# Performance work log

Measured on AMD Instinct MI355X. Metric: run time of the kernel, lower is better.

Reference implementation:

```python
import jax, jax.numpy as jnp
import numpy as np
import math

L, B, T, E, HQ, HKV, V = 6, 4, 1024, 1024, 16, 4, 32000
D = E // HQ          # head dim = 64
G = HQ // HKV        # group size = 4
EKV = E // G         # kv proj dim = 256


def setup_inputs() -> dict:
    key = jax.random.key(0)
    ks = jax.random.split(key, 16)
    def n(k, shape):
        return jax.random.normal(k, shape, jnp.float32) * 0.02
    return dict(
        idx=jax.random.randint(ks[0], (B, T), 0, V),
        wte=n(ks[1], (V, E)),
        Wq=n(ks[2], (L, E, E)), bq=jnp.zeros((L, E), jnp.float32),
        Wk=n(ks[3], (L, EKV, E)), bk=jnp.zeros((L, EKV), jnp.float32),
        Wv=n(ks[4], (L, EKV, E)), bv=jnp.zeros((L, EKV), jnp.float32),
        Wo=n(ks[5], (L, E, E)), bo=jnp.zeros((L, E), jnp.float32),
        ln1_w=jnp.ones((L, E), jnp.float32), ln1_b=jnp.zeros((L, E), jnp.float32),
        ln2_w=jnp.ones((L, E), jnp.float32), ln2_b=jnp.zeros((L, E), jnp.float32),
        Wfc=n(ks[6], (L, 4 * E, E)), bfc=jnp.zeros((L, 4 * E), jnp.float32),
        Wproj=n(ks[7], (L, E, 4 * E)), bproj=jnp.zeros((L, E), jnp.float32),
        lnf_w=jnp.ones((E,), jnp.float32), lnf_b=jnp.zeros((E,), jnp.float32),
        lm_head=n(ks[8], (V, E)),
    )


def _ln(x, w, b):
    m = x.mean(-1, keepdims=True)
    v = ((x - m) ** 2).mean(-1, keepdims=True)
    return (x - m) * jax.lax.rsqrt(v + 1e-5) * w + b


def _gelu_new(x):
    c = math.sqrt(2.0 / math.pi)
    return 0.5 * x * (1.0 + jnp.tanh(c * (x + 0.044715 * x ** 3)))


def _rope_tables(t, d):
    # positions start at 1; thetas = base^(-2*(i-1)/d), i = 1..d/2
    pos = jnp.arange(1, t + 1, dtype=jnp.float32)
    thetas = 10000.0 ** (-2.0 * jnp.arange(d // 2, dtype=jnp.float32) / d)
    ang = pos[:, None] * thetas                      # [t, d/2]
    cos = jnp.concatenate([jnp.cos(ang)] * 2, -1)    # [t, d]
    sin = jnp.concatenate([jnp.sin(ang)] * 2, -1)
    return cos, sin


def _apply_rope(x, cos, sin):
    # x: [b, h, t, d]; x_cos = x; x_sin = concat(-right, left)
    x1, x2 = x[..., : D // 2], x[..., D // 2:]
    return x * cos + jnp.concatenate([-x2, x1], -1) * sin


def _gpt_forward(idx, wte, Wq, bq, Wk, bk, Wv, bv, Wo, bo,
                 ln1_w, ln1_b, ln2_w, ln2_b, Wfc, bfc, Wproj, bproj,
                 lnf_w, lnf_b, lm_head):
    cos, sin = _rope_tables(T, D)
    mask = jnp.tril(jnp.ones((T, T), bool))          # causal
    scale = 1.0 / math.sqrt(D)
    x = wte[idx]                                     # [B, T, E]
    for l in range(L):
        h = _ln(x, ln1_w[l], ln1_b[l])
        q = (h @ Wq[l].T + bq[l]).reshape(B, T, HQ, D).transpose(0, 2, 1, 3)
        k = (h @ Wk[l].T + bk[l]).reshape(B, T, HKV, D).transpose(0, 2, 1, 3)
        v = (h @ Wv[l].T + bv[l]).reshape(B, T, HKV, D).transpose(0, 2, 1, 3)
        q = _apply_rope(q, cos, sin)
        k = _apply_rope(k, cos, sin)
        q = q.reshape(B, HKV, G, T, D)               # kv-major head grouping
        att = jnp.einsum('bhgqd,bhkd->bhgqk', q, k) * scale
        att = jnp.where(mask, att, -jnp.inf)
        att = jax.nn.softmax(att, axis=-1)
        y = jnp.einsum('bhgqk,bhkd->bhgqd', att, v)
        y = y.transpose(0, 3, 1, 2, 4).reshape(B, T, E)   # b q (h g d)
        x = x + (y @ Wo[l].T + bo[l])
        h2 = _ln(x, ln2_w[l], ln2_b[l])
        ff = _gelu_new(h2 @ Wfc[l].T + bfc[l]) @ Wproj[l].T + bproj[l]
        x = x + ff
    x = _ln(x, lnf_w, lnf_b)
    return x @ lm_head.T                             # [B, T, V] logits


def reference(idx, wte, Wq, bq, Wk, bk, Wv, bv, Wo, bo,
              ln1_w, ln1_b, ln2_w, ln2_b, Wfc, bfc, Wproj, bproj,
              lnf_w, lnf_b, lm_head):
    return _gpt_forward(idx, wte, Wq, bq, Wk, bk, Wv, bv, Wo, bo,
                        ln1_w, ln1_b, ln2_w, ln2_b, Wfc, bfc, Wproj, bproj,
                        lnf_w, lnf_b, lm_head)
```

## Files before the change

kernel.cpp:

```cpp
#include <hip/hip_runtime.h>

#define Lz 6
#define Bz 4
#define Tz 1024
#define Ez 1024
#define HQz 16
#define HKVz 4
#define Dz 64
#define EKVz 256
#define Vz 32000
#define FFz 4096
#define QKVz 1536

typedef __attribute__((ext_vector_type(4))) float f32x4;
typedef __attribute__((ext_vector_type(8))) short short8;
typedef unsigned short ushort_t;

__device__ inline ushort_t f2b(float f) {
  union { float f; unsigned u; } x; x.f = f;
  unsigned r = x.u + 0x7fffu + ((x.u >> 16) & 1u);
  return (ushort_t)(r >> 16);
}
__device__ inline float b2f(ushort_t u) {
  union { unsigned u; float f; } x; x.u = ((unsigned)u) << 16;
  return x.f;
}
__device__ inline unsigned packbf(float lo, float hi) {
  return (unsigned)f2b(lo) | ((unsigned)f2b(hi) << 16);
}

__device__ inline void gload16(const void* g, void* l) {
  __builtin_amdgcn_global_load_lds(
      (const __attribute__((address_space(1))) void*)g,
      (__attribute__((address_space(3))) void*)l, 16, 0, 0);
}

template<int BIAS, int GELU, int WF32>
__global__ __launch_bounds__(512, 2) void gemm_bt256(
    const ushort_t* __restrict__ A, const ushort_t* __restrict__ Bw,
    const float* __restrict__ bias,
    float* __restrict__ Cf, ushort_t* __restrict__ Cb,
    int M, int N, int K)
{
  __shared__ ushort_t sA[2][2][128 * 64];
  __shared__ ushort_t sB[2][2][128 * 64];
  const int tid = threadIdx.x;
  const int lane = tid & 63, wid = tid >> 6;
  const int wr = wid >> 2, wc = wid & 3;
  const int l15 = lane & 15, l4 = lane >> 4;

  const int gx = gridDim.x;
  const int nwg = gx * gridDim.y;
  const int orig = blockIdx.y * gx + blockIdx.x;
  const int qq = nwg >> 3, rr = nwg & 7;
  const int xcd = orig & 7, loc = orig >> 3;
  const int swz = (xcd < rr) ? (xcd * (qq + 1) + loc)
                             : (rr * (qq + 1) + (xcd - rr) * qq + loc);
  const int bm = swz % gx, bn = swz / gx;

  const int NT = K >> 6;

  auto stage = [&](const ushort_t* src, int row_base, int k0, ushort_t* dst) {
#pragma unroll
    for (int i = 0; i < 2; ++i) {
      int s = i * 512 + tid;
      int row = s >> 3, jp = s & 7;
      int jlog = jp ^ (row & 7);
      gload16(src + (size_t)(row_base + row) * K + k0 + jlog * 8, (char*)dst + s * 16);
    }
  };

  stage(A,  bm * 256,       0, &sA[0][0][0]);
  stage(A,  bm * 256 + 128, 0, &sA[0][1][0]);
  stage(Bw, bn * 256,       0, &sB[0][0][0]);
  stage(Bw, bn * 256 + 128, 0, &sB[0][1][0]);
  stage(A,  bm * 256,       64, &sA[1][0][0]);
  stage(A,  bm * 256 + 128, 64, &sA[1][1][0]);
  stage(Bw, bn * 256,       64, &sB[1][0][0]);
  stage(Bw, bn * 256 + 128, 64, &sB[1][1][0]);
  asm volatile("s_waitcnt vmcnt(8)" ::: "memory");
  __builtin_amdgcn_sched_barrier(0);
  __builtin_amdgcn_s_barrier();
  __builtin_amdgcn_sched_barrier(0);

  f32x4 acc[8][4] = {};
  const int axc = l15 & 7;

  for (int t = 0; t < NT; ++t) {
    const int b = t & 1;
    const ushort_t* pA = &sA[b][wr][0];
    const ushort_t* pB = &sB[b][wc >> 1][(wc & 1) * 64 * 64];
    short8 aF[8][2], bF[4][2];

#pragma unroll
    for (int mt = 0; mt < 4; ++mt)
#pragma unroll
      for (int ks = 0; ks < 2; ++ks)
        aF[mt][ks] = *(const short8*)&pA[(mt * 16 + l15) * 64 + (((ks << 2) + l4) ^ axc) * 8];
#pragma unroll
    for (int nt = 0; nt < 4; ++nt)
      bF[nt][0] = *(const short8*)&pB[(nt * 16 + l15) * 64 + (l4 ^ axc) * 8];
    __builtin_amdgcn_s_setprio(1);
#pragma unroll
    for (int mt = 0; mt < 4; ++mt)
#pragma unroll
      for (int nt = 0; nt < 4; ++nt)
        acc[mt][nt] = __builtin_amdgcn_mfma_f32_16x16x32_bf16(aF[mt][0], bF[nt][0], acc[mt][nt], 0, 0, 0);
    __builtin_amdgcn_s_setprio(0);

#pragma unroll
    for (int mt = 4; mt < 8; ++mt)
#pragma unroll
      for (int ks = 0; ks < 2; ++ks)
        aF[mt][ks] = *(const short8*)&pA[(mt * 16 + l15) * 64 + (((ks << 2) + l4) ^ axc) * 8];
#pragma unroll
    for (int nt = 0; nt < 4; ++nt)
      bF[nt][1] = *(const short8*)&pB[(nt * 16 + l15) * 64 + ((4 + l4) ^ axc) * 8];
    __builtin_amdgcn_s_setprio(1);
#pragma unroll
    for (int mt = 0; mt < 4; ++mt)
#pragma unroll
      for (int nt = 0; nt < 4; ++nt)
        acc[mt][nt] = __builtin_amdgcn_mfma_f32_16x16x32_bf16(aF[mt][1], bF[nt][1], acc[mt][nt], 0, 0, 0);
    __builtin_amdgcn_s_setprio(0);

    asm volatile("s_waitcnt lgkmcnt(0)" ::: "memory");
    __builtin_amdgcn_sched_barrier(0);
    __builtin_amdgcn_s_barrier();
    __builtin_amdgcn_sched_barrier(0);

    const bool pf = (t + 2 < NT);
    if (pf) {
      const int k2 = (t + 2) << 6;
      stage(Bw, bn * 256,       k2, &sB[b][0][0]);
      stage(Bw, bn * 256 + 128, k2, &sB[b][1][0]);
    }
    __builtin_amdgcn_s_setprio(1);
#pragma unroll
    for (int mt = 4; mt < 8; ++mt)
#pragma unroll
      for (int nt = 0; nt < 4; ++nt)
        acc[mt][nt] = __builtin_amdgcn_mfma_f32_16x16x32_bf16(aF[mt][0], bF[nt][0], acc[mt][nt], 0, 0, 0);
    __builtin_amdgcn_s_setprio(0);

    if (pf) {
      const int k2 = (t + 2) << 6;
      stage(A, bm * 256,       k2, &sA[b][0][0]);
      stage(A, bm * 256 + 128, k2, &sA[b][1][0]);
    }
    __builtin_amdgcn_s_setprio(1);
#pragma unroll
    for (int mt = 4; mt < 8; ++mt)
#pragma unroll
      for (int nt = 0; nt < 4; ++nt)
        acc[mt][nt] = __builtin_amdgcn_mfma_f32_16x16x32_bf16(aF[mt][1], bF[nt][1], acc[mt][nt], 0, 0, 0);
    __builtin_amdgcn_s_setprio(0);

    if (t + 1 < NT) {
      if (pf) { asm volatile("s_waitcnt vmcnt(8)" ::: "memory"); }
      else    { asm volatile("s_waitcnt vmcnt(0)" ::: "memory"); }
      __builtin_amdgcn_sched_barrier(0);
      __builtin_amdgcn_s_barrier();
      __builtin_amdgcn_sched_barrier(0);
    }
  }

#pragma unroll
  for (int mt = 0; mt < 8; ++mt) {
#pragma unroll
    for (int nt = 0; nt < 4; ++nt) {
      const int col = bn * 256 + wc * 64 + nt * 16 + l15;
#pragma unroll
      for (int i = 0; i < 4; ++i) {
        const int row = bm * 256 + wr * 128 + mt * 16 + l4 * 4 + i;
        float v = acc[mt][nt][i];
        if (BIAS) v += bias[col];
        if (GELU) {
          float x = v;
          v = 0.5f * x * (1.f + tanhf(0.7978845608028654f * (x + 0.044715f * x * x * x)));
        }
        const size_t o = (size_t)row * N + col;
        if (WF32) Cf[o] = v; else Cb[o] = f2b(v);
      }
    }
  }
}

template<int BIAS, int RES, int GELU, int WF32, int WBF16, int ROPE>
__global__ __launch_bounds__(256) void gemm_bt(
    const ushort_t* __restrict__ A, const ushort_t* __restrict__ Bw,
    const float* __restrict__ bias, const float* __restrict__ res,
    float* __restrict__ Cf, ushort_t* __restrict__ Cb,
    const float2* __restrict__ tab,
    int M, int N, int K)
{
  __shared__ ushort_t sA[2][128 * 32];
  __shared__ ushort_t sB[2][128 * 32];
  const int tid = threadIdx.x;
  const int lane = tid & 63, wid = tid >> 6;
  const int wm = wid >> 1, wn = wid & 1;
  const int l15 = lane & 15, l4 = lane >> 4;

  const int gx = gridDim.x;
  const int nwg = gx * gridDim.y;
  const int orig = blockIdx.y * gx + blockIdx.x;
  const int qq = nwg >> 3, rr = nwg & 7;
  const int xcd = orig & 7, loc = orig >> 3;
  const int swz = (xcd < rr) ? (xcd * (qq + 1) + loc)
                             : (rr * (qq + 1) + (xcd - rr) * qq + loc);
  const int bm = swz % gx, bn = swz / gx;

  f32x4 acc[4][4] = {};
  const int nK = K >> 5;

#pragma unroll
  for (int j = 0; j < 2; ++j) {
    int s = wid * 128 + j * 64 + lane;
    int row = s >> 2, c8 = (s & 3) << 3;
    gload16(A + (size_t)(bm * 128 + row) * K + c8, (char*)&sA[0][0] + s * 16);
    gload16(Bw + (size_t)(bn * 128 + row) * K + c8, (char*)&sB[0][0] + s * 16);
  }
  __syncthreads();

  int cur = 0;
  for (int kt = 0; kt < nK; ++kt) {
    if (kt + 1 < nK) {
      const int k0 = (kt + 1) << 5;
      const int nb = cur ^ 1;
#pragma unroll
      for (int j = 0; j < 2; ++j) {
        int s = wid * 128 + j * 64 + lane;
        int row = s >> 2, c8 = (s & 3) << 3;
        gload16(A + (size_t)(bm * 128 + row) * K + k0 + c8, (char*)&sA[nb][0] + s * 16);
        gload16(Bw + (size_t)(bn * 128 + row) * K + k0 + c8, (char*)&sB[nb][0] + s * 16);
      }
    }
    short8 aF[4], bF[4];
#pragma unroll
    for (int mt = 0; mt < 4; ++mt)
      aF[mt] = *(const short8*)&sA[cur][(wm * 64 + mt * 16 + l15) * 32 + l4 * 8];
#pragma unroll
    for (int nt = 0; nt < 4; ++nt)
      bF[nt] = *(const short8*)&sB[cur][(wn * 64 + nt * 16 + l15) * 32 + l4 * 8];
#pragma unroll
    for (int mt = 0; mt < 4; ++mt)
#pragma unroll
      for (int nt = 0; nt < 4; ++nt)
        acc[mt][nt] = __builtin_amdgcn_mfma_f32_16x16x32_bf16(aF[mt], bF[nt], acc[mt][nt], 0, 0, 0);
    __syncthreads();
    cur ^= 1;
  }

  if (ROPE) {
    const int col0 = bn * 128 + wn * 64;
    const bool isv = (col0 >= 1280);
#pragma unroll
    for (int mt = 0; mt < 4; ++mt) {
#pragma unroll
      for (int i = 0; i < 4; ++i) {
        const int row = bm * 128 + wm * 64 + mt * 16 + l4 * 4 + i;
        const int t = row & (Tz - 1);
        if (isv) {
#pragma unroll
          for (int nt = 0; nt < 4; ++nt) {
            const int col = col0 + nt * 16 + l15;
            Cb[(size_t)row * N + col] = f2b(acc[mt][nt][i] + bias[col]);
          }
        } else {
#pragma unroll
          for (int nt = 0; nt < 2; ++nt) {
            const int col = col0 + nt * 16 + l15;
            const int jj = nt * 16 + l15;
            const float2 cs = tab[t * 32 + jj];
            const float x1 = acc[mt][nt][i] + bias[col];
            const float x2 = acc[mt][nt + 2][i] + bias[col + 32];
            Cb[(size_t)row * N + col]      = f2b(x1 * cs.x - x2 * cs.y);
            Cb[(size_t)row * N + col + 32] = f2b(x2 * cs.x + x1 * cs.y);
          }
        }
      }
    }
    return;
  }

#pragma unroll
  for (int mt = 0; mt < 4; ++mt) {
#pragma unroll
    for (int nt = 0; nt < 4; ++nt) {
      const int col = bn * 128 + wn * 64 + nt * 16 + l15;
#pragma unroll
      for (int i = 0; i < 4; ++i) {
        const int row = bm * 128 + wm * 64 + mt * 16 + l4 * 4 + i;
        float v = acc[mt][nt][i];
        if (BIAS) v += bias[col];
        if (GELU) {
          float t = v;
          v = 0.5f * t * (1.f + tanhf(0.7978845608028654f * (t + 0.044715f * t * t * t)));
        }
        const size_t o = (size_t)row * N + col;
        if (RES) v += res[o];
        if (WF32) Cf[o] = v;
        if (WBF16) Cb[o] = f2b(v);
      }
    }
  }
}

__global__ __launch_bounds__(256, 4) void attn_k(
    const ushort_t* __restrict__ qkv, const ushort_t* __restrict__ vt,
    ushort_t* __restrict__ y)
{
  __shared__ ushort_t sK[2][64 * 64];
  __shared__ ushort_t sV[2][64 * 64];
  __shared__ unsigned sPu[4][512];
  const int qt = blockIdx.x;
  const int bh = blockIdx.y;
  const int b = bh >> 4, h = bh & 15, hk = h >> 2;
  const int tid = threadIdx.x, lane = tid & 63, wid = tid >> 6;
  const int l15 = lane & 15, l4 = lane >> 4;
  const int qrow0 = qt * 64 + wid * 16;
  const int qg = qrow0 + l15;
  const int xr = l15 & 7;

  short8 aQ[2];
#pragma unroll
  for (int ks = 0; ks < 2; ++ks)
    aQ[ks] = *(const short8*)&qkv[(size_t)(b * Tz + qrow0 + l15) * QKVz + h * 64 + ks * 32 + l4 * 8];

  float m = -1e30f, lsum = 0.f;
  f32x4 o[4] = {};

  const int ntile = qt + 1;

#pragma unroll
  for (int j = 0; j < 2; ++j) {
    int s = wid * 128 + j * 64 + lane;
    int row = s >> 3, jp = s & 7, jlog = jp ^ (row & 7);
    gload16(qkv + (size_t)(b * Tz + row) * QKVz + Ez + hk * 64 + jlog * 8, (char*)&sK[0][0] + s * 16);
    gload16(vt + (size_t)((b * HKVz + hk) * 64 + row) * Tz + jlog * 8, (char*)&sV[0][0] + s * 16);
  }

  for (int t = 0; t < ntile; ++t) {
    asm volatile("s_waitcnt vmcnt(0)" ::: "memory");
    __syncthreads();
    if (t + 1 < ntile) {
      const int nb = (t + 1) & 1;
#pragma unroll
      for (int j = 0; j < 2; ++j) {
        int s = wid * 128 + j * 64 + lane;
        int row = s >> 3, jp = s & 7, jlog = jp ^ (row & 7);
        gload16(qkv + (size_t)(b * Tz + (t + 1) * 64 + row) * QKVz + Ez + hk * 64 + jlog * 8,
                (char*)&sK[nb][0] + s * 16);
        gload16(vt + (size_t)((b * HKVz + hk) * 64 + row) * Tz + (t + 1) * 64 + jlog * 8,
                (char*)&sV[nb][0] + s * 16);
      }
    }
    const ushort_t* K = &sK[t & 1][0];
    const ushort_t* V = &sV[t & 1][0];

    f32x4 sacc[4] = {};
#pragma unroll
    for (int nt = 0; nt < 4; ++nt) {
#pragma unroll
      for (int ks = 0; ks < 2; ++ks) {
        short8 aK = *(const short8*)&K[(nt * 16 + l15) * 64 + (((ks << 2) + l4) ^ xr) * 8];
        sacc[nt] = __builtin_amdgcn_mfma_f32_16x16x32_bf16(aK, aQ[ks], sacc[nt], 0, 0, 0);
      }
    }

    float sv[4][4];
    float pmax = -1e30f;
#pragma unroll
    for (int nt = 0; nt < 4; ++nt)
#pragma unroll
      for (int i = 0; i < 4; ++i) {
        int key = t * 64 + nt * 16 + l4 * 4 + i;
        float s = sacc[nt][i] * 0.125f;
        if (key > qg) s = -1e30f;
        sv[nt][i] = s;
        pmax = fmaxf(pmax, s);
      }
    pmax = fmaxf(pmax, __shfl_xor(pmax, 16));
    pmax = fmaxf(pmax, __shfl_xor(pmax, 32));
    const float mnew = fmaxf(m, pmax);
    const float corr = __expf(m - mnew);
    float psum = 0.f;
#pragma unroll
    for (int nt = 0; nt < 4; ++nt)
#pragma unroll
      for (int i = 0; i < 4; ++i) {
        float p = __expf(sv[nt][i] - mnew);
        sv[nt][i] = p;
        psum += p;
      }
    psum += __shfl_xor(psum, 16);
    psum += __shfl_xor(psum, 32);
    lsum = lsum * corr + psum;
    m = mnew;
#pragma unroll
    for (int dt = 0; dt < 4; ++dt) o[dt] *= corr;

#pragma unroll
    for (int nt = 0; nt < 4; ++nt) {
      uint2 u;
      u.x = packbf(sv[nt][0], sv[nt][1]);
      u.y = packbf(sv[nt][2], sv[nt][3]);
      *(uint2*)&sPu[wid][l15 * 32 + (((nt * 2 + (l4 >> 1)) ^ xr) << 2) + ((l4 & 1) << 1)] = u;
    }
    short8 aP[2];
#pragma unroll
    for (int ks = 0; ks < 2; ++ks)
      aP[ks] = *(const short8*)&sPu[wid][l15 * 32 + ((((ks << 2) + l4) ^ xr) << 2)];

#pragma unroll
    for (int dt = 0; dt < 4; ++dt) {
#pragma unroll
      for (int ks = 0; ks < 2; ++ks) {
        short8 aV = *(const short8*)&V[(dt * 16 + l15) * 64 + (((ks << 2) + l4) ^ xr) * 8];
        o[dt] = __builtin_amdgcn_mfma_f32_16x16x32_bf16(aV, aP[ks], o[dt], 0, 0, 0);
      }
    }
  }

  const float inv = 1.f / lsum;
  const size_t yrow = (size_t)(b * Tz + qrow0 + l15) * Ez + h * 64;
#pragma unroll
  for (int dt = 0; dt < 4; ++dt) {
    ushort4 w;
    w.x = f2b(o[dt][0] * inv);
    w.y = f2b(o[dt][1] * inv);
    w.z = f2b(o[dt][2] * inv);
    w.w = f2b(o[dt][3] * inv);
    *(ushort4*)&y[yrow + dt * 16 + l4 * 4] = w;
  }
}

__global__ __launch_bounds__(256) void vtrans_k(
    const ushort_t* __restrict__ qkv, ushort_t* __restrict__ vt)
{
  __shared__ ushort_t tile[64][72];
  const int tt = blockIdx.x, bh = blockIdx.y;
  const int b = bh >> 2, hk = bh & 3;
  const int tid = threadIdx.x;
  {
    const int r = tid >> 2, c0 = (tid & 3) * 16;
    const ushort_t* src = qkv + (size_t)(b * Tz + tt * 64 + r) * QKVz + 1280 + hk * 64 + c0;
    *(short8*)&tile[r][c0] = *(const short8*)src;
    *(short8*)&tile[r][c0 + 8] = *(const short8*)(src + 8);
  }
  __syncthreads();
  {
    const int d = tid >> 2, t0 = (tid & 3) * 16;
    ushort_t* dst = vt + (size_t)((b * HKVz + hk) * 64 + d) * Tz + tt * 64 + t0;
    short8 o0, o1;
#pragma unroll
    for (int ii = 0; ii < 8; ++ii) { o0[ii] = (short)tile[t0 + ii][d]; o1[ii] = (short)tile[t0 + 8 + ii][d]; }
    *(short8*)dst = o0;
    *(short8*)(dst + 8) = o1;
  }
}

__global__ __launch_bounds__(256) void ln_bf16(
    const float* __restrict__ x, const float* __restrict__ w,
    const float* __restrict__ b, ushort_t* __restrict__ out)
{
  __shared__ float red[8];
  const int row = blockIdx.x, tid = threadIdx.x;
  float4 vv = *(const float4*)&x[(size_t)row * Ez + tid * 4];
  float s = vv.x + vv.y + vv.z + vv.w;
  float sq = vv.x * vv.x + vv.y * vv.y + vv.z * vv.z + vv.w * vv.w;
#pragma unroll
  for (int off = 1; off < 64; off <<= 1) { s += __shfl_xor(s, off); sq += __shfl_xor(sq, off); }
  if ((tid & 63) == 0) { red[(tid >> 6) * 2] = s; red[(tid >> 6) * 2 + 1] = sq; }
  __syncthreads();
  const float ts = red[0] + red[2] + red[4] + red[6];
  const float tq = red[1] + red[3] + red[5] + red[7];
  const float mean = ts * (1.f / Ez);
  const float var = tq * (1.f / Ez) - mean * mean;
  const float rstd = rsqrtf(var + 1e-5f);
  float4 wv = *(const float4*)&w[tid * 4];
  float4 bv = *(const float4*)&b[tid * 4];
  ushort4 ov;
  ov.x = f2b((vv.x - mean) * rstd * wv.x + bv.x);
  ov.y = f2b((vv.y - mean) * rstd * wv.y + bv.y);
  ov.z = f2b((vv.z - mean) * rstd * wv.z + bv.z);
  ov.w = f2b((vv.w - mean) * rstd * wv.w + bv.w);
  *(ushort4*)&out[(size_t)row * Ez + tid * 4] = ov;
}

__global__ __launch_bounds__(256) void embed_k(
    const int* __restrict__ idx, const float* __restrict__ wte, float* __restrict__ x)
{
  int i = blockIdx.x * 256 + threadIdx.x;
  int row = i >> 8, c = (i & 255) << 2;
  *(float4*)&x[(size_t)row * Ez + c] = *(const float4*)&wte[(size_t)idx[row] * Ez + c];
}

__global__ __launch_bounds__(256) void cvt_bf16(
    const float* __restrict__ in, ushort_t* __restrict__ out, int n)
{
  int i = (blockIdx.x * 256 + threadIdx.x) * 4;
  if (i >= n) return;
  float4 v = *(const float4*)&in[i];
  ushort4 o;
  o.x = f2b(v.x); o.y = f2b(v.y); o.z = f2b(v.z); o.w = f2b(v.w);
  *(ushort4*)&out[i] = o;
}

__global__ __launch_bounds__(256) void cvt_layer(
    const float* __restrict__ Wq, const float* __restrict__ Wk,
    const float* __restrict__ Wv, const float* __restrict__ Wo_,
    const float* __restrict__ Wfc_, const float* __restrict__ Wpj_,
    ushort_t* __restrict__ wqkv, ushort_t* __restrict__ wo,
    ushort_t* __restrict__ wfc, ushort_t* __restrict__ wpj)
{
  int i = (blockIdx.x * 256 + threadIdx.x) * 4;
  const float* src; ushort_t* dst; int off;
  if (i < 1048576)       { src = Wq;   dst = wqkv;           off = i; }
  else if (i < 1310720)  { src = Wk;   dst = wqkv + 1048576; off = i - 1048576; }
  else if (i < 1572864)  { src = Wv;   dst = wqkv + 1310720; off = i - 1310720; }
  else if (i < 2621440)  { src = Wo_;  dst = wo;             off = i - 1572864; }
  else if (i < 6815744)  { src = Wfc_; dst = wfc;            off = i - 2621440; }
  else                   { src = Wpj_; dst = wpj;            off = i - 6815744; }
  float4 v = *(const float4*)&src[off];
  ushort4 o;
  o.x = f2b(v.x); o.y = f2b(v.y); o.z = f2b(v.z); o.w = f2b(v.w);
  *(ushort4*)&dst[off] = o;
}

__global__ __launch_bounds__(256) void rope_tab_k(float2* __restrict__ tab)
{
  int i = blockIdx.x * 256 + threadIdx.x;
  int t = i >> 5, j = i & 31;
  float theta = powf(10000.0f, -(float)j / 32.0f);
  float ang = (float)(t + 1) * theta;
  tab[i] = make_float2(cosf(ang), sinf(ang));
}

__global__ __launch_bounds__(256) void biascat_all(
    const float* __restrict__ bq, const float* __restrict__ bk,
    const float* __restrict__ bv, float* __restrict__ out)
{
  int i = blockIdx.x * 256 + threadIdx.x;
  int l = i / QKVz, j = i - l * QKVz;
  float v = (j < Ez) ? bq[l * Ez + j]
          : ((j < Ez + EKVz) ? bk[l * EKVz + j - Ez] : bv[l * EKVz + j - Ez - EKVz]);
  out[i] = v;
}

template<int BIAS, int RES, int GELU, int WF32, int WBF16, int ROPE = 0>
static void launch_gemm(const ushort_t* A, const ushort_t* Bw, const float* bias,
                        const float* res, float* Cf, ushort_t* Cb, const float* tab,
                        int M, int N, int K, hipStream_t s)
{
  dim3 g(M / 128, N / 128);
  gemm_bt<BIAS, RES, GELU, WF32, WBF16, ROPE><<<g, 256, 0, s>>>(
      A, Bw, bias, res, Cf, Cb, (const float2*)tab, M, N, K);
}

extern "C" void kernel_launch(void* const* d_in, const int* in_sizes, int n_in,
                              void* d_out, int out_size, void* d_ws, size_t ws_size,
                              hipStream_t stream)
{
  (void)in_sizes; (void)n_in; (void)out_size; (void)ws_size;
  const int*   idx   = (const int*)d_in[0];
  const float* wte   = (const float*)d_in[1];
  const float* Wq    = (const float*)d_in[2];
  const float* bq    = (const float*)d_in[3];
  const float* Wk    = (const float*)d_in[4];
  const float* bk    = (const float*)d_in[5];
  const float* Wv    = (const float*)d_in[6];
  const float* bv    = (const float*)d_in[7];
  const float* Wo    = (const float*)d_in[8];
  const float* bo    = (const float*)d_in[9];
  const float* ln1w  = (const float*)d_in[10];
  const float* ln1b  = (const float*)d_in[11];
  const float* ln2w  = (const float*)d_in[12];
  const float* ln2b  = (const float*)d_in[13];
  const float* Wfc   = (const float*)d_in[14];
  const float* bfc   = (const float*)d_in[15];
  const float* Wproj = (const float*)d_in[16];
  const float* bproj = (const float*)d_in[17];
  const float* lnfw  = (const float*)d_in[18];
  const float* lnfb  = (const float*)d_in[19];
  const float* lmh   = (const float*)d_in[20];
  float* out = (float*)d_out;

  char* ws = (char*)d_ws;
  size_t off = 0;
  auto alloc = [&](size_t bytes) -> void* {
    void* p = ws + off;
    off += (bytes + 255) & ~(size_t)255;
    return p;
  };
  ushort_t* wbuf  = (ushort_t*)alloc((size_t)Vz * Ez * 2);
  float*    x     = (float*)alloc((size_t)Bz * Tz * Ez * 4);
  ushort_t* hb    = (ushort_t*)alloc((size_t)Bz * Tz * Ez * 2);
  ushort_t* qkvb  = (ushort_t*)alloc((size_t)Bz * Tz * QKVz * 2);
  ushort_t* vtb   = (ushort_t*)alloc((size_t)Bz * HKVz * 64 * Tz * 2);
  ushort_t* yb    = (ushort_t*)alloc((size_t)Bz * Tz * Ez * 2);
  ushort_t* ffb   = (ushort_t*)alloc((size_t)Bz * Tz * FFz * 2);
  float*    tab   = (float*)alloc((size_t)Tz * 32 * 2 * 4);
  float*    qbia  = (float*)alloc((size_t)Lz * QKVz * 4);

  ushort_t* wqkv = wbuf;
  ushort_t* wo   = wqkv + (size_t)QKVz * Ez;
  ushort_t* wfc  = wo + (size_t)Ez * Ez;
  ushort_t* wpj  = wfc + (size_t)FFz * Ez;

  const int M = Bz * Tz;

  rope_tab_k<<<Tz * 32 / 256, 256, 0, stream>>>((float2*)tab);
  biascat_all<<<Lz * QKVz / 256, 256, 0, stream>>>(bq, bk, bv, qbia);
  embed_k<<<Bz * Tz, 256, 0, stream>>>(idx, wte, x);

  for (int l = 0; l < Lz; ++l) {
    ln_bf16<<<M, 256, 0, stream>>>(x, ln1w + l * Ez, ln1b + l * Ez, hb);
    cvt_layer<<<10752, 256, 0, stream>>>(
        Wq + (size_t)l * Ez * Ez, Wk + (size_t)l * EKVz * Ez, Wv + (size_t)l * EKVz * Ez,
        Wo + (size_t)l * Ez * Ez, Wfc + (size_t)l * FFz * Ez, Wproj + (size_t)l * Ez * FFz,
        wqkv, wo, wfc, wpj);
    launch_gemm<1, 0, 0, 0, 1, 1>(hb, wqkv, qbia + l * QKVz, nullptr, nullptr, qkvb, tab,
                                  M, QKVz, Ez, stream);
    vtrans_k<<<dim3(Tz / 64, Bz * HKVz), 256, 0, stream>>>(qkvb, vtb);
    attn_k<<<dim3(Tz / 64, Bz * HQz), 256, 0, stream>>>(qkvb, vtb, yb);
    launch_gemm<1, 1, 0, 1, 0>(yb, wo, bo + l * Ez, x, x, nullptr, nullptr, M, Ez, Ez, stream);
    ln_bf16<<<M, 256, 0, stream>>>(x, ln2w + l * Ez, ln2b + l * Ez, hb);
    {
      dim3 g(M / 256, FFz / 256);
      gemm_bt256<1, 1, 0><<<g, 512, 0, stream>>>(hb, wfc, bfc + l * FFz, nullptr, ffb, M, FFz, Ez);
    }
    launch_gemm<1, 1, 0, 1, 0>(ffb, wpj, bproj + l * Ez, x, x, nullptr, nullptr, M, Ez, FFz, stream);
  }
  ln_bf16<<<M, 256, 0, stream>>>(x, lnfw, lnfb, hb);
  cvt_bf16<<<(Vz * Ez / 4 + 255) / 256, 256, 0, stream>>>(lmh, wbuf, Vz * Ez);
  {
    dim3 g(M / 256, Vz / 256);
    gemm_bt256<0, 0, 1><<<g, 512, 0, stream>>>(hb, wbuf, nullptr, out, nullptr, M, Vz, Ez);
  }
}
```

Baseline: 1.945 ms.

## Add 8-wave pipelined LM-head GEMM and reverse attention tile order

```diff
diff --git a/kernel.cpp b/kernel.cpp
--- a/kernel.cpp
+++ b/kernel.cpp
@@ -186,6 +186,156 @@
   }
 }
 
+__global__ __launch_bounds__(512, 2) void gemm_lmh8(
+    const ushort_t* __restrict__ A, const ushort_t* __restrict__ Bw,
+    float* __restrict__ Cf, int M, int N, int K)
+{
+  __shared__ ushort_t sA[2][2][128 * 64];
+  __shared__ ushort_t sB[2][2][128 * 64];
+  const int tid = threadIdx.x;
+  const int lane = tid & 63, wid = tid >> 6;
+  const int wr = wid >> 2, wc = wid & 3;
+  const int l15 = lane & 15, l4 = lane >> 4;
+  const int axc = l15 & 7;
+
+  const int gx = gridDim.x;
+  const int nwg = gx * gridDim.y;
+  const int orig = blockIdx.y * gx + blockIdx.x;
+  const int qq = nwg >> 3, rr = nwg & 7;
+  const int xcd = orig & 7, loc = orig >> 3;
+  const int swz = (xcd < rr) ? (xcd * (qq + 1) + loc)
+                             : (rr * (qq + 1) + (xcd - rr) * qq + loc);
+  const int bm = swz % gx, bn = swz / gx;
+
+  const int NT = K >> 6, NI = NT >> 1;
+
+  auto stage = [&](const ushort_t* src, int row_base, int k0, ushort_t* dst) {
+#pragma unroll
+    for (int i = 0; i < 2; ++i) {
+      int s = i * 512 + tid;
+      int row = s >> 3, jp = s & 7;
+      int jlog = jp ^ (row & 7);
+      gload16(src + (size_t)(row_base + row) * K + k0 + jlog * 8, (char*)dst + s * 16);
+    }
+  };
+
+  f32x4 acc[8][4] = {};
+  short8 aF[4][2], bF[4][2];
+
+#define FEN asm volatile("" ::: "memory")
+#define BARR do { FEN; __builtin_amdgcn_s_barrier(); FEN; } while (0)
+#define LGKM0 do { asm volatile("s_waitcnt lgkmcnt(0)" ::: "memory"); \
+                   __builtin_amdgcn_sched_barrier(0); } while (0)
+#define LGKM8 asm volatile("s_waitcnt lgkmcnt(8)" ::: "memory")
+#define VMW(nimm) asm volatile("s_waitcnt vmcnt(" #nimm ")" ::: "memory")
+#define LDA4(base, mt0) do { \
+  const ushort_t* _p = (base); \
+  _Pragma("unroll") for (int _j = 0; _j < 4; ++_j) \
+  _Pragma("unroll") for (int _k = 0; _k < 2; ++_k) \
+    aF[_j][_k] = *(const short8*)&_p[(((mt0) + _j) * 16 + l15) * 64 + ((((_k << 2) + l4)) ^ axc) * 8]; \
+} while (0)
+#define LDB2(base, nt0) do { \
+  const ushort_t* _p = (base); \
+  _Pragma("unroll") for (int _j = 0; _j < 2; ++_j) \
+  _Pragma("unroll") for (int _k = 0; _k < 2; ++_k) \
+    bF[(nt0) + _j][_k] = *(const short8*)&_p[(((nt0) + _j) * 16 + l15) * 64 + ((((_k << 2) + l4)) ^ axc) * 8]; \
+} while (0)
+#define MM16(mt0, nt0) do { \
+  __builtin_amdgcn_s_setprio(1); \
+  _Pragma("unroll") for (int _j = 0; _j < 4; ++_j) \
+  _Pragma("unroll") for (int _n = 0; _n < 2; ++_n) \
+  _Pragma("unroll") for (int _k = 0; _k < 2; ++_k) \
+    acc[(mt0) + _j][(nt0) + _n] = __builtin_amdgcn_mfma_f32_16x16x32_bf16( \
+        aF[_j][_k], bF[(nt0) + _n][_k], acc[(mt0) + _j][(nt0) + _n], 0, 0, 0); \
+  __builtin_amdgcn_s_setprio(0); \
+} while (0)
+
+  stage(A,  bm * 256,       0,  &sA[0][0][0]);
+  stage(A,  bm * 256 + 128, 0,  &sA[0][1][0]);
+  stage(Bw, bn * 256,       0,  &sB[0][0][0]);
+  stage(Bw, bn * 256 + 128, 0,  &sB[0][1][0]);
+  stage(Bw, bn * 256,       64, &sB[1][0][0]);
+  stage(Bw, bn * 256 + 128, 64, &sB[1][1][0]);
+  VMW(4);
+  BARR;
+
+  for (int i = 0; i < NI; ++i) {
+    const bool pf = (2 * i + 2 < NT);
+    const int kA  = (2 * i + 1) << 6;
+    const int kB0 = (2 * i + 2) << 6;
+    const int kB1 = (2 * i + 3) << 6;
+    const ushort_t* pA0 = &sA[0][wr][0];
+    const ushort_t* pA1 = &sA[1][wr][0];
+    const ushort_t* pB0 = &sB[0][wc >> 1][(wc & 1) * 64 * 64];
+    const ushort_t* pB1 = &sB[1][wc >> 1][(wc & 1) * 64 * 64];
+
+    stage(A, bm * 256, kA, &sA[1][0][0]);
+    LDA4(pA0, 0); LDB2(pB0, 0);
+    LGKM8;
+    BARR; LGKM0;
+    MM16(0, 0);
+    BARR;
+    stage(A, bm * 256 + 128, kA, &sA[1][1][0]);
+    LDB2(pB0, 2);
+    BARR; LGKM0;
+    MM16(0, 2);
+    BARR;
+    if (pf) stage(Bw, bn * 256, kB0, &sB[0][0][0]);
+    LDA4(pA0, 4);
+    BARR; LGKM0;
+    MM16(4, 0);
+    BARR;
+    if (pf) { stage(Bw, bn * 256 + 128, kB0, &sB[0][1][0]); VMW(4); }
+    else    { VMW(0); }
+    BARR;
+    MM16(4, 2);
+    BARR;
+    if (pf) stage(A, bm * 256, kB0, &sA[0][0][0]);
+    LDA4(pA1, 0); LDB2(pB1, 0);
+    LGKM8;
+    BARR; LGKM0;
+    MM16(0, 0);
+    BARR;
+    if (pf) stage(A, bm * 256 + 128, kB0, &sA[0][1][0]);
+    LDB2(pB1, 2);
+    BARR; LGKM0;
+    MM16(0, 2);
+    BARR;
+    if (pf) stage(Bw, bn * 256, kB1, &sB[1][0][0]);
+    LDA4(pA1, 4);
+    BARR; LGKM0;
+    MM16(4, 0);
+    BARR;
+    if (pf) { stage(Bw, bn * 256 + 128, kB1, &sB[1][1][0]); VMW(4); }
+    else    { VMW(0); }
+    BARR;
+    MM16(4, 2);
+    BARR;
+  }
+
+#undef FEN
+#undef BARR
+#undef LGKM0
+#undef LGKM8
+#undef VMW
+#undef LDA4
+#undef LDB2
+#undef MM16
+
+#pragma unroll
+  for (int mt = 0; mt < 8; ++mt) {
+#pragma unroll
+    for (int nt = 0; nt < 4; ++nt) {
+      const int col = bn * 256 + wc * 64 + nt * 16 + l15;
+#pragma unroll
+      for (int i = 0; i < 4; ++i) {
+        const int row = bm * 256 + wr * 128 + mt * 16 + l4 * 4 + i;
+        Cf[(size_t)row * N + col] = acc[mt][nt][i];
+      }
+    }
+  }
+}
+
 template<int BIAS, int RES, int GELU, int WF32, int WBF16, int ROPE>
 __global__ __launch_bounds__(256) void gemm_bt(
     const ushort_t* __restrict__ A, const ushort_t* __restrict__ Bw,
@@ -313,7 +463,7 @@
   __shared__ ushort_t sK[2][64 * 64];
   __shared__ ushort_t sV[2][64 * 64];
   __shared__ unsigned sPu[4][512];
-  const int qt = blockIdx.x;
+  const int qt = (Tz / 64 - 1) - blockIdx.x;
   const int bh = blockIdx.y;
   const int b = bh >> 4, h = bh & 15, hk = h >> 2;
   const int tid = threadIdx.x, lane = tid & 63, wid = tid >> 6;
@@ -636,6 +786,6 @@
   cvt_bf16<<<(Vz * Ez / 4 + 255) / 256, 256, 0, stream>>>(lmh, wbuf, Vz * Ez);
   {
     dim3 g(M / 256, Vz / 256);
-    gemm_bt256<0, 0, 1><<<g, 512, 0, stream>>>(hb, wbuf, nullptr, out, nullptr, M, Vz, Ez);
-  }
-}
+    gemm_lmh8<<<g, 512, 0, stream>>>(hb, wbuf, out, M, Vz, Ez);
+  }
+}
```

Result: slower. 1.993 ms (+2.4%).
